# Kernel optimization log

Hardware: AMD Instinct MI355X
Metric: run time of the kernel (lower is better)

Reference implementation:

```python
import jax, jax.numpy as jnp
import numpy as np

SHAPELET_SIZE = 64
NUM_SHAPELETS = 128
IN_CHANNELS = 8


def setup_inputs() -> dict:
    key = jax.random.key(0)
    k1, k2 = jax.random.split(key)
    x = jax.random.normal(k1, (64, IN_CHANNELS, 2048), dtype=jnp.float32)
    shapelets = jax.random.normal(k2, (IN_CHANNELS, NUM_SHAPELETS, SHAPELET_SIZE), dtype=jnp.float32)
    return {"x": x, "shapelets": shapelets}


def _znorm(s):
    # Z-normalize along the time-step axis (dim 2), matching Znormalize_dim(shapelets, 2)
    mu = jnp.mean(s, axis=2, keepdims=True)
    sd = jnp.std(s, axis=2, keepdims=True)
    return (s - mu) / sd


def reference(x, shapelets):
    # x: (N, C, L); shapelets: (C, K, S)
    S = shapelets.shape[-1]
    N, C, L = x.shape
    W = L - S + 1
    # unfold(2, S, 1): sliding windows -> (N, C, W, S)
    idx = jnp.arange(W)[:, None] + jnp.arange(S)[None, :]  # (W, S)
    xw = x[:, :, idx]  # (N, C, W, S)
    sh = _znorm(shapelets)  # (C, K, S)
    # Euclidean cdist via ||a||^2 + ||b||^2 - 2 a.b (avoids (N,C,W,K,S) blowup)
    sq_x = jnp.sum(xw * xw, axis=-1)          # (N, C, W)
    sq_s = jnp.sum(sh * sh, axis=-1)          # (C, K)
    cross = jnp.einsum('ncws,cks->ncwk', xw, sh)  # (N, C, W, K)
    d2 = sq_x[..., None] + sq_s[None, :, None, :] - 2.0 * cross
    d = jnp.sqrt(jnp.maximum(d2, 1e-12))      # (N, C, W, K)
    # sum over channels, then global min over windows -> (N, 1, K)
    dsum = jnp.sum(d, axis=1)                 # (N, W, K)
    out = jnp.min(dsum, axis=1)[:, None, :]   # (N, 1, K)
    return out
```

## Files before the change

### kernel.cpp

```cpp
#include <hip/hip_runtime.h>
#include <hip/hip_bf16.h>
#include <math.h>

#define C 8
#define K 128
#define S 64
#define L 2048
#define NB 64
#define W (L - S + 1)
#define TW 128
#define NTW 16
#define XCS 208
#define XFS 200

typedef __attribute__((ext_vector_type(8))) short bf16x8;
typedef __attribute__((ext_vector_type(4))) float f32x4;

__device__ __forceinline__ unsigned short f2bf(float f) {
  unsigned int u = __float_as_uint(f);
  u += 0x7FFFu + ((u >> 16) & 1u);
  return (unsigned short)(u >> 16);
}

__device__ __forceinline__ unsigned int pkbf(float a, float b) {
  __hip_bfloat162 h = __float22bfloat162_rn(make_float2(a, b));
  return *reinterpret_cast<unsigned int*>(&h);
}

__global__ __launch_bounds__(256) void prep_kernel(const float* __restrict__ sh,
                                                   unsigned short* __restrict__ shzB,
                                                   float* __restrict__ out) {
  int tid = blockIdx.x * 256 + threadIdx.x;
  if (tid < NB * K) out[tid] = __int_as_float(0x7F800000);
  int gid = blockIdx.x * 4 + (threadIdx.x >> 6);
  int lane = threadIdx.x & 63;
  float v = sh[(size_t)gid * S + lane];
  float s1 = v, s2 = v * v;
#pragma unroll
  for (int off = 32; off > 0; off >>= 1) {
    s1 += __shfl_down(s1, off);
    s2 += __shfl_down(s2, off);
  }
  s1 = __shfl(s1, 0);
  s2 = __shfl(s2, 0);
  float mu = s1 * (1.0f / S);
  float sd = sqrtf(fmaxf(s2 * (1.0f / S) - mu * mu, 0.0f));
  float z = (v - mu) / sd;
  int c = gid >> 7, k = gid & (K - 1), s = lane;
  int idx = c * 8192 + (k >> 6) * 4096 + ((((k >> 4) & 3) * 2) + (s >> 5)) * 512 +
            ((((s >> 3) & 3) * 16 + (k & 15)) * 8) + (s & 7);
  shzB[idx] = f2bf(-2.0f * z);
}

__global__ __launch_bounds__(256, 3) void main_kernel(const float* __restrict__ x,
                                                      const unsigned short* __restrict__ shzB,
                                                      int* __restrict__ out) {
  __shared__ __align__(16) unsigned short xcop[C][8][XCS];
  __shared__ __align__(16) float sqx[C][TW];
  __shared__ __align__(16) float xf[C][XFS];

  const int t = threadIdx.x;
  const int lane = t & 63;
  const int wave = t >> 6;
  const int wgrp = wave & 1;
  const int kgrp = wave >> 1;
  const int col = lane & 15;
  const int quad = lane >> 4;
  const int n = blockIdx.y;
  const int w0 = blockIdx.x * TW;
  const float* xn = x + (size_t)n * C * L;
  const unsigned short* bw = shzB + kgrp * 4096 + lane * 8;

  float* xfp = &xf[0][0];
#pragma unroll
  for (int cc = 0; cc < 2; ++cc) {
    const int c = wave * 2 + cc;
    const int e = lane * 4;
    float4 v; v.x = v.y = v.z = v.w = 0.0f;
    if (lane < 48) {
      int g = w0 + e;
      if (g + 3 < L) {
        v = *(const float4*)(xn + c * L + g);
      } else {
        v.x = (g + 0 < L) ? xn[c * L + g + 0] : 0.0f;
        v.y = (g + 1 < L) ? xn[c * L + g + 1] : 0.0f;
        v.z = (g + 2 < L) ? xn[c * L + g + 2] : 0.0f;
        v.w = (g + 3 < L) ? xn[c * L + g + 3] : 0.0f;
      }
    }
    if (lane < 50) *(float4*)&xfp[c * XFS + e] = v;
  }
  __syncthreads();

#pragma unroll
  for (int cc = 0; cc < 2; ++cc) {
    const int cb = wave * 2 + cc;
    const int rb = lane >> 3;
    const int c8 = lane & 7;
    const float* xr = xfp + cb * XFS;
#pragma unroll
    for (int j = 0; j < 12; ++j) {
      int i = (c8 + j * 8) * 2;
      *(unsigned int*)&xcop[cb][rb][i] = pkbf(xr[i + rb], xr[i + rb + 1]);
    }
  }
#pragma unroll
  for (int cc = 0; cc < 2; ++cc) {
    const int c = wave * 2 + cc, wl = lane * 2;
    const float* xr = xfp + c * XFS;
    float p0 = 0.f, p1 = 0.f, p2 = 0.f, p3 = 0.f;
#pragma unroll
    for (int si = 0; si < S; si += 4) {
      float v0 = xr[wl + si], v1 = xr[wl + si + 1], v2 = xr[wl + si + 2], v3 = xr[wl + si + 3];
      p0 = fmaf(v0, v0, p0); p1 = fmaf(v1, v1, p1);
      p2 = fmaf(v2, v2, p2); p3 = fmaf(v3, v3, p3);
    }
    float s0 = 64.0f + (p0 + p1) + (p2 + p3);
    sqx[c][wl] = s0;
    float a = xr[wl + S], b = xr[wl];
    sqx[c][wl + 1] = s0 + a * a - b * b;
  }
  __syncthreads();

  const f32x4 z4 = {0.0f, 0.0f, 0.0f, 0.0f};
  f32x4 dsum[4][4];
#pragma unroll
  for (int kt = 0; kt < 4; ++kt)
#pragma unroll
    for (int wt = 0; wt < 4; ++wt) dsum[kt][wt] = z4;

  const int r8 = col & 7;
  const int abase = wgrp * 64 + (col - r8) + quad * 8;

  for (int c = 0; c < C; ++c) {
    bf16x8 Bc[8];
#pragma unroll
    for (int i = 0; i < 8; ++i)
      Bc[i] = *(const bf16x8*)(bw + c * 8192 + i * 512);

    const unsigned short* xc = &xcop[c][r8][0];
#pragma unroll
    for (int wt = 0; wt < 4; ++wt) {
      f32x4 ai = *(const f32x4*)&sqx[c][wgrp * 64 + wt * 16 + quad * 4];
      bf16x8 x0 = *(const bf16x8*)(xc + abase + wt * 16);
      bf16x8 x1 = *(const bf16x8*)(xc + abase + wt * 16 + 32);
      f32x4 a0 = __builtin_amdgcn_mfma_f32_16x16x32_bf16(x0, Bc[0], ai, 0, 0, 0);
      f32x4 a1 = __builtin_amdgcn_mfma_f32_16x16x32_bf16(x0, Bc[2], ai, 0, 0, 0);
      f32x4 a2 = __builtin_amdgcn_mfma_f32_16x16x32_bf16(x0, Bc[4], ai, 0, 0, 0);
      f32x4 a3 = __builtin_amdgcn_mfma_f32_16x16x32_bf16(x0, Bc[6], ai, 0, 0, 0);
      a0 = __builtin_amdgcn_mfma_f32_16x16x32_bf16(x1, Bc[1], a0, 0, 0, 0);
      a1 = __builtin_amdgcn_mfma_f32_16x16x32_bf16(x1, Bc[3], a1, 0, 0, 0);
      a2 = __builtin_amdgcn_mfma_f32_16x16x32_bf16(x1, Bc[5], a2, 0, 0, 0);
      a3 = __builtin_amdgcn_mfma_f32_16x16x32_bf16(x1, Bc[7], a3, 0, 0, 0);
#pragma unroll
      for (int i = 0; i < 4; ++i) {
        dsum[0][wt][i] += __builtin_amdgcn_sqrtf(fmaxf(a0[i], 0.0f));
        dsum[1][wt][i] += __builtin_amdgcn_sqrtf(fmaxf(a1[i], 0.0f));
        dsum[2][wt][i] += __builtin_amdgcn_sqrtf(fmaxf(a2[i], 0.0f));
        dsum[3][wt][i] += __builtin_amdgcn_sqrtf(fmaxf(a3[i], 0.0f));
      }
    }
  }

  const float INF = __int_as_float(0x7F800000);
  const int wbase = w0 + wgrp * 64;
#pragma unroll
  for (int kt = 0; kt < 4; ++kt) {
    float mv = INF;
#pragma unroll
    for (int wt = 0; wt < 4; ++wt)
#pragma unroll
      for (int i = 0; i < 4; ++i) {
        int w = wbase + wt * 16 + quad * 4 + i;
        mv = (w < W) ? fminf(mv, dsum[kt][wt][i]) : mv;
      }
    mv = fminf(mv, __shfl_xor(mv, 16));
    mv = fminf(mv, __shfl_xor(mv, 32));
    if (quad == 0)
      atomicMin(&out[n * K + kgrp * 64 + kt * 16 + col], __float_as_int(mv));
  }
}

extern "C" void kernel_launch(void* const* d_in, const int* in_sizes, int n_in,
                              void* d_out, int out_size, void* d_ws, size_t ws_size,
                              hipStream_t stream) {
  const float* x = (const float*)d_in[0];
  const float* sh = (const float*)d_in[1];
  float* out = (float*)d_out;
  unsigned short* shzB = (unsigned short*)d_ws;

  prep_kernel<<<256, 256, 0, stream>>>(sh, shzB, out);
  main_kernel<<<dim3(NTW, NB), 256, 0, stream>>>(x, shzB, (int*)out);
}
```

Before: 87.92 us.

## Software-pipeline MFMA and sqrt epilogue across channels, lower occupancy to 2

The channel loop is restructured so the MFMAs for channel c are issued after the sqrt/accumulate of channel c-1's results. This lets the matrix unit and the VALU work in parallel instead of the sqrt waiting on freshly produced accumulators. A separate 64-float result buffer p is kept live, which raises register pressure. The launch bound is relaxed from 3 to 2 blocks per SIMD to make room, at the cost of occupancy.

```diff
diff --git a/kernel.cpp b/kernel.cpp
--- a/kernel.cpp
+++ b/kernel.cpp
@@ -52,7 +52,7 @@
   shzB[idx] = f2bf(-2.0f * z);
 }
 
-__global__ __launch_bounds__(256, 3) void main_kernel(const float* __restrict__ x,
+__global__ __launch_bounds__(256, 2) void main_kernel(const float* __restrict__ x,
                                                       const unsigned short* __restrict__ shzB,
                                                       int* __restrict__ out) {
   __shared__ __align__(16) unsigned short xcop[C][8][XCS];
@@ -132,35 +132,78 @@
   const int r8 = col & 7;
   const int abase = wgrp * 64 + (col - r8) + quad * 8;
 
-  for (int c = 0; c < C; ++c) {
+  f32x4 p[4][4];
+
+  {
+    bf16x8 Bc[8];
+#pragma unroll
+    for (int i = 0; i < 8; ++i)
+      Bc[i] = *(const bf16x8*)(bw + i * 512);
+    const unsigned short* xc = &xcop[0][r8][0];
+#pragma unroll
+    for (int wt = 0; wt < 4; ++wt) {
+      f32x4 ai = *(const f32x4*)&sqx[0][wgrp * 64 + wt * 16 + quad * 4];
+      bf16x8 x0 = *(const bf16x8*)(xc + abase + wt * 16);
+      bf16x8 x1 = *(const bf16x8*)(xc + abase + wt * 16 + 32);
+      p[0][wt] = __builtin_amdgcn_mfma_f32_16x16x32_bf16(x0, Bc[0], ai, 0, 0, 0);
+      p[1][wt] = __builtin_amdgcn_mfma_f32_16x16x32_bf16(x0, Bc[2], ai, 0, 0, 0);
+      p[2][wt] = __builtin_amdgcn_mfma_f32_16x16x32_bf16(x0, Bc[4], ai, 0, 0, 0);
+      p[3][wt] = __builtin_amdgcn_mfma_f32_16x16x32_bf16(x0, Bc[6], ai, 0, 0, 0);
+      p[0][wt] = __builtin_amdgcn_mfma_f32_16x16x32_bf16(x1, Bc[1], p[0][wt], 0, 0, 0);
+      p[1][wt] = __builtin_amdgcn_mfma_f32_16x16x32_bf16(x1, Bc[3], p[1][wt], 0, 0, 0);
+      p[2][wt] = __builtin_amdgcn_mfma_f32_16x16x32_bf16(x1, Bc[5], p[2][wt], 0, 0, 0);
+      p[3][wt] = __builtin_amdgcn_mfma_f32_16x16x32_bf16(x1, Bc[7], p[3][wt], 0, 0, 0);
+    }
+  }
+
+  for (int c = 1; c < C; ++c) {
     bf16x8 Bc[8];
 #pragma unroll
     for (int i = 0; i < 8; ++i)
       Bc[i] = *(const bf16x8*)(bw + c * 8192 + i * 512);
 
     const unsigned short* xc = &xcop[c][r8][0];
+    bf16x8 xa0[4], xa1[4];
+    f32x4 aiv[4];
 #pragma unroll
     for (int wt = 0; wt < 4; ++wt) {
-      f32x4 ai = *(const f32x4*)&sqx[c][wgrp * 64 + wt * 16 + quad * 4];
-      bf16x8 x0 = *(const bf16x8*)(xc + abase + wt * 16);
-      bf16x8 x1 = *(const bf16x8*)(xc + abase + wt * 16 + 32);
-      f32x4 a0 = __builtin_amdgcn_mfma_f32_16x16x32_bf16(x0, Bc[0], ai, 0, 0, 0);
-      f32x4 a1 = __builtin_amdgcn_mfma_f32_16x16x32_bf16(x0, Bc[2], ai, 0, 0, 0);
-      f32x4 a2 = __builtin_amdgcn_mfma_f32_16x16x32_bf16(x0, Bc[4], ai, 0, 0, 0);
-      f32x4 a3 = __builtin_amdgcn_mfma_f32_16x16x32_bf16(x0, Bc[6], ai, 0, 0, 0);
-      a0 = __builtin_amdgcn_mfma_f32_16x16x32_bf16(x1, Bc[1], a0, 0, 0, 0);
-      a1 = __builtin_amdgcn_mfma_f32_16x16x32_bf16(x1, Bc[3], a1, 0, 0, 0);
-      a2 = __builtin_amdgcn_mfma_f32_16x16x32_bf16(x1, Bc[5], a2, 0, 0, 0);
-      a3 = __builtin_amdgcn_mfma_f32_16x16x32_bf16(x1, Bc[7], a3, 0, 0, 0);
+      xa0[wt] = *(const bf16x8*)(xc + abase + wt * 16);
+      xa1[wt] = *(const bf16x8*)(xc + abase + wt * 16 + 32);
+      aiv[wt] = *(const f32x4*)&sqx[c][wgrp * 64 + wt * 16 + quad * 4];
+    }
+
+#pragma unroll
+    for (int wt = 0; wt < 4; ++wt)
 #pragma unroll
       for (int i = 0; i < 4; ++i) {
-        dsum[0][wt][i] += __builtin_amdgcn_sqrtf(fmaxf(a0[i], 0.0f));
-        dsum[1][wt][i] += __builtin_amdgcn_sqrtf(fmaxf(a1[i], 0.0f));
-        dsum[2][wt][i] += __builtin_amdgcn_sqrtf(fmaxf(a2[i], 0.0f));
-        dsum[3][wt][i] += __builtin_amdgcn_sqrtf(fmaxf(a3[i], 0.0f));
+        dsum[0][wt][i] += __builtin_amdgcn_sqrtf(fmaxf(p[0][wt][i], 0.0f));
+        dsum[1][wt][i] += __builtin_amdgcn_sqrtf(fmaxf(p[1][wt][i], 0.0f));
+        dsum[2][wt][i] += __builtin_amdgcn_sqrtf(fmaxf(p[2][wt][i], 0.0f));
+        dsum[3][wt][i] += __builtin_amdgcn_sqrtf(fmaxf(p[3][wt][i], 0.0f));
       }
-    }
-  }
+
+#pragma unroll
+    for (int wt = 0; wt < 4; ++wt) {
+      p[0][wt] = __builtin_amdgcn_mfma_f32_16x16x32_bf16(xa0[wt], Bc[0], aiv[wt], 0, 0, 0);
+      p[1][wt] = __builtin_amdgcn_mfma_f32_16x16x32_bf16(xa0[wt], Bc[2], aiv[wt], 0, 0, 0);
+      p[2][wt] = __builtin_amdgcn_mfma_f32_16x16x32_bf16(xa0[wt], Bc[4], aiv[wt], 0, 0, 0);
+      p[3][wt] = __builtin_amdgcn_mfma_f32_16x16x32_bf16(xa0[wt], Bc[6], aiv[wt], 0, 0, 0);
+      p[0][wt] = __builtin_amdgcn_mfma_f32_16x16x32_bf16(xa1[wt], Bc[1], p[0][wt], 0, 0, 0);
+      p[1][wt] = __builtin_amdgcn_mfma_f32_16x16x32_bf16(xa1[wt], Bc[3], p[1][wt], 0, 0, 0);
+      p[2][wt] = __builtin_amdgcn_mfma_f32_16x16x32_bf16(xa1[wt], Bc[5], p[2][wt], 0, 0, 0);
+      p[3][wt] = __builtin_amdgcn_mfma_f32_16x16x32_bf16(xa1[wt], Bc[7], p[3][wt], 0, 0, 0);
+    }
+  }
+
+#pragma unroll
+  for (int wt = 0; wt < 4; ++wt)
+#pragma unroll
+    for (int i = 0; i < 4; ++i) {
+      dsum[0][wt][i] += __builtin_amdgcn_sqrtf(fmaxf(p[0][wt][i], 0.0f));
+      dsum[1][wt][i] += __builtin_amdgcn_sqrtf(fmaxf(p[1][wt][i], 0.0f));
+      dsum[2][wt][i] += __builtin_amdgcn_sqrtf(fmaxf(p[2][wt][i], 0.0f));
+      dsum[3][wt][i] += __builtin_amdgcn_sqrtf(fmaxf(p[3][wt][i], 0.0f));
+    }
 
   const float INF = __int_as_float(0x7F800000);
   const int wbase = w0 + wgrp * 64;
```

Result: no change. 87.59 us (-0.4%).
